# Kernel tuning notes

Hardware: AMD Instinct MI355X
Metric: run time of the kernel (lower is better)

The kernel has to match this reference:

```python
import jax, jax.numpy as jnp
import numpy as np

SEQ, D_IN, D_OUT = 8192, 1024, 1024

def setup_inputs() -> dict:
    key = jax.random.key(0)
    kx, kq, kk, kv = jax.random.split(key, 4)
    scale = 1.0 / np.sqrt(D_IN)
    return {
        "x": jax.random.normal(kx, (SEQ, D_IN), dtype=jnp.float32),
        "Wq": jax.random.normal(kq, (D_OUT, D_IN), dtype=jnp.float32) * scale,
        "Wk": jax.random.normal(kk, (D_OUT, D_IN), dtype=jnp.float32) * scale,
        "Wv": jax.random.normal(kv, (D_OUT, D_IN), dtype=jnp.float32) * scale,
    }

def reference(x, Wq, Wk, Wv):
    # nn.Linear: y = x @ W.T (no bias)
    q = x @ Wq.T            # [S, d_out]
    k = x @ Wk.T            # [S, d_out]
    v = x @ Wv.T            # [S, d_out]
    d_k = k.shape[-1]
    scores = (q @ k.T) / jnp.sqrt(jnp.float32(d_k))   # [S, S]
    attn = jax.nn.softmax(scores, axis=-1)
    return attn @ v         # [S, d_out]
```

## Files before the change

### kernel.cpp

```cpp
#include <hip/hip_runtime.h>

typedef unsigned short ushort_t;
typedef __attribute__((ext_vector_type(8))) __bf16 bf16x8;
typedef __attribute__((ext_vector_type(4))) float f32x4;

#define SEQ 8192
#define DIN 1024
#define DOUT 1024

#define OM_BF16 0
#define OM_F32  1
#define OM_EXP  2
#define OM_NORM 3

__device__ __forceinline__ ushort_t f2bf(float f) {
  union { float f; unsigned u; } c; c.f = f;
  unsigned u = c.u;
  return (ushort_t)((u + 0x7fffu + ((u >> 16) & 1u)) >> 16);
}

__device__ __forceinline__ void async16(ushort_t* lds, const ushort_t* g) {
  __builtin_amdgcn_global_load_lds(
      (__attribute__((address_space(1))) void*)g,
      (__attribute__((address_space(3))) void*)lds, 16, 0, 0);
}

__global__ __launch_bounds__(256) void cvt_all_kernel(
    const float* __restrict__ x, const float* __restrict__ wq,
    const float* __restrict__ wk, const float* __restrict__ wv,
    ushort_t* __restrict__ xb, ushort_t* __restrict__ wqkb,
    ushort_t* __restrict__ wvb) {
  int b = blockIdx.x;
  const float* src;
  ushort_t* dst;
  int idx;
  if (b < 8192) {
    src = x; dst = xb; idx = b * 256 + threadIdx.x;
  } else {
    int r = b - 8192;
    int w = r >> 10;
    idx = (r & 1023) * 256 + threadIdx.x;
    if (w == 0)      { src = wq; dst = wqkb; }
    else if (w == 1) { src = wk; dst = wqkb + DOUT * DIN; }
    else             { src = wv; dst = wvb; }
  }
  float4 f = ((const float4*)src)[idx];
  ushort4 o;
  o.x = f2bf(f.x); o.y = f2bf(f.y); o.z = f2bf(f.z); o.w = f2bf(f.w);
  ((ushort4*)dst)[idx] = o;
}

__global__ __launch_bounds__(256) void rowsum_inv_kernel(const float* __restrict__ rsp,
                                                         float* __restrict__ invrs) {
  int r = blockIdx.x * 256 + threadIdx.x;
  float s = 0.f;
  #pragma unroll
  for (int p2 = 0; p2 < 64; ++p2) s += rsp[p2 * SEQ + r];
  invrs[r] = 1.0f / s;
}

template <int OUTMODE, int SWZ, int BK>
__global__ __launch_bounds__(256) void gemm_bt(const ushort_t* __restrict__ A,
                                               const ushort_t* __restrict__ B,
                                               void* __restrict__ C,
                                               int lda, int ldb, int ldc,
                                               int K, float scale,
                                               float* __restrict__ rsp,
                                               const float* __restrict__ invrs) {
  constexpr int CPR = BK / 8;
  constexpr int NI = BK / 16;
  __shared__ ushort_t As[128 * BK];
  __shared__ ushort_t Bs[128 * BK];
  const int t = threadIdx.x;
  const int lane = t & 63;
  const int wave = t >> 6;
  const int wr = wave >> 1, wc = wave & 1;
  const int quad = lane >> 4, r16 = lane & 15;

  int mt, nt;
  if (SWZ == 1) {
    mt = blockIdx.x * (gridDim.y >> 3) + (blockIdx.y >> 3);
    nt = blockIdx.y & 7;
  } else {
    mt = blockIdx.y;
    nt = blockIdx.x;
  }
  const int rowBase = mt * 128;
  const int colBase = nt * 128;

  unsigned offA[NI], offB[NI];
  #pragma unroll
  for (int i = 0; i < NI; ++i) {
    int c = t + i * 256;
    int row = c / CPR;
    int kq = c & (CPR - 1);
    int kqs = (kq & ~7) | ((kq & 7) ^ (row & 7));
    offA[i] = (unsigned)((rowBase + row) * lda + kqs * 8);
    offB[i] = (unsigned)((colBase + row) * ldb + kqs * 8);
  }

  f32x4 acc[4][4] = {};

  const int nk = K / BK;
  for (int kt = 0; kt < nk; ++kt) {
    #pragma unroll
    for (int i = 0; i < NI; ++i) {
      async16(&As[(t + i * 256) * 8], A + offA[i]); offA[i] += BK;
      async16(&Bs[(t + i * 256) * 8], B + offB[i]); offB[i] += BK;
    }
    __syncthreads();
    #pragma unroll
    for (int ks = 0; ks < BK / 32; ++ks) {
      bf16x8 af[4], bfr[4];
      #pragma unroll
      for (int mi = 0; mi < 4; ++mi) {
        int row = wr * 64 + mi * 16 + r16;
        int kq = ks * 4 + quad;
        int c = row * CPR + ((kq & ~7) | ((kq & 7) ^ (row & 7)));
        af[mi] = *(const bf16x8*)&As[c * 8];
      }
      #pragma unroll
      for (int ni = 0; ni < 4; ++ni) {
        int row = wc * 64 + ni * 16 + r16;
        int kq = ks * 4 + quad;
        int c = row * CPR + ((kq & ~7) | ((kq & 7) ^ (row & 7)));
        bfr[ni] = *(const bf16x8*)&Bs[c * 8];
      }
      #pragma unroll
      for (int mi = 0; mi < 4; ++mi)
        #pragma unroll
        for (int ni = 0; ni < 4; ++ni)
          acc[mi][ni] = __builtin_amdgcn_mfma_f32_16x16x32_bf16(af[mi], bfr[ni],
                                                                acc[mi][ni], 0, 0, 0);
    }
    __syncthreads();
  }

  float iv[4][4];
  if (OUTMODE == OM_NORM) {
    #pragma unroll
    for (int mi = 0; mi < 4; ++mi)
      #pragma unroll
      for (int r = 0; r < 4; ++r)
        iv[mi][r] = invrs[rowBase + wr * 64 + mi * 16 + quad * 4 + r];
  }

  float psum[4][4];
  if (OUTMODE == OM_EXP) {
    #pragma unroll
    for (int mi = 0; mi < 4; ++mi)
      #pragma unroll
      for (int r = 0; r < 4; ++r) psum[mi][r] = 0.f;
  }

  #pragma unroll
  for (int mi = 0; mi < 4; ++mi)
    #pragma unroll
    for (int ni = 0; ni < 4; ++ni)
      #pragma unroll
      for (int r = 0; r < 4; ++r) {
        int grow = rowBase + wr * 64 + mi * 16 + quad * 4 + r;
        int gcol = colBase + wc * 64 + ni * 16 + r16;
        float a = acc[mi][ni][r];
        if (OUTMODE == OM_F32) {
          ((float*)C)[(size_t)grow * ldc + gcol] = a * scale;
        } else if (OUTMODE == OM_BF16) {
          ((ushort_t*)C)[(size_t)grow * ldc + gcol] = f2bf(a * scale);
        } else if (OUTMODE == OM_EXP) {
          float e = exp2f(a * scale);
          psum[mi][r] += e;
          ((ushort_t*)C)[(size_t)grow * ldc + gcol] = f2bf(e);
        } else {
          ((float*)C)[(size_t)grow * ldc + gcol] = a * iv[mi][r];
        }
      }

  if (OUTMODE == OM_EXP) {
    float* lds_rs = (float*)As;
    #pragma unroll
    for (int mi = 0; mi < 4; ++mi)
      #pragma unroll
      for (int r = 0; r < 4; ++r) {
        float s = psum[mi][r];
        s += __shfl_xor(s, 1, 64);
        s += __shfl_xor(s, 2, 64);
        s += __shfl_xor(s, 4, 64);
        s += __shfl_xor(s, 8, 64);
        if (r16 == 0)
          lds_rs[wc * 128 + wr * 64 + mi * 16 + quad * 4 + r] = s;
      }
    __syncthreads();
    if (t < 128)
      rsp[(size_t)nt * SEQ + rowBase + t] = lds_rs[t] + lds_rs[128 + t];
  }
}

extern "C" void kernel_launch(void* const* d_in, const int* in_sizes, int n_in,
                              void* d_out, int out_size, void* d_ws, size_t ws_size,
                              hipStream_t stream) {
  const float* x  = (const float*)d_in[0];
  const float* Wq = (const float*)d_in[1];
  const float* Wk = (const float*)d_in[2];
  const float* Wv = (const float*)d_in[3];
  float* out = (float*)d_out;

  char* p = (char*)d_ws;
  ushort_t* xb   = (ushort_t*)p; p += (size_t)SEQ * DIN * 2;
  ushort_t* wqkb = (ushort_t*)p; p += (size_t)2 * DOUT * DIN * 2;
  ushort_t* wvb  = (ushort_t*)p; p += (size_t)DOUT * DIN * 2;
  ushort_t* qkb  = (ushort_t*)p; p += (size_t)SEQ * 2 * DOUT * 2;
  ushort_t* vtb  = (ushort_t*)p; p += (size_t)DOUT * SEQ * 2;
  float*    rsp  = (float*)p;    p += (size_t)64 * SEQ * 4;
  float*    irs  = (float*)p;    p += (size_t)SEQ * 4;
  ushort_t* Sb   = (ushort_t*)p; p += (size_t)SEQ * SEQ * 2;

  cvt_all_kernel<<<8192 + 3 * 1024, 256, 0, stream>>>(x, Wq, Wk, Wv, xb, wqkb, wvb);

  dim3 blk(256);
  gemm_bt<OM_BF16, 0, 64><<<dim3(2048 / 128, SEQ / 128), blk, 0, stream>>>(
      xb, wqkb, qkb, DIN, DIN, 2 * DOUT, DIN, 1.0f, nullptr, nullptr);

  gemm_bt<OM_BF16, 0, 128><<<dim3(SEQ / 128, DOUT / 128), blk, 0, stream>>>(
      wvb, xb, vtb, DIN, DIN, SEQ, DIN, 1.0f, nullptr, nullptr);

  gemm_bt<OM_EXP, 0, 64><<<dim3(SEQ / 128, SEQ / 128), blk, 0, stream>>>(
      qkb, qkb + DOUT, Sb, 2 * DOUT, 2 * DOUT, SEQ, DIN,
      0.03125f * 1.44269504f, rsp, nullptr);

  rowsum_inv_kernel<<<SEQ / 256, blk, 0, stream>>>(rsp, irs);

  gemm_bt<OM_NORM, 1, 128><<<dim3(DOUT / 128, SEQ / 128), blk, 0, stream>>>(
      Sb, vtb, out, SEQ, SEQ, DOUT, SEQ, 1.0f, nullptr, irs);
}
```

Before: 478.0 us.

## Merge QK and V projections into one launch, use packed bf16 conversion

Merges the two projection GEMMs (QK and transposed V) into a single launch of 1536 blocks. The V projection now uses BK=64 instead of 128. Bf16 conversion uses the hardware packed cvt instruction where available, both in the input cast kernel and in the GEMM epilogues. The epilogue loop is restructured so the row multiplier is computed once per row. The aim is to remove one launch and its tail, and to cut the ALU cost of the bf16 rounding. Stores stay scalar 16-bit, and rounding behaviour may differ slightly.

```diff
diff --git a/kernel.cpp b/kernel.cpp
--- a/kernel.cpp
+++ b/kernel.cpp
@@ -13,10 +13,30 @@
 #define OM_EXP  2
 #define OM_NORM 3
 
+#if defined(__has_builtin)
+#if __has_builtin(__builtin_amdgcn_cvt_pk_bf16_f32)
+#define HAVE_PK_BF16 1
+#endif
+#endif
+#ifndef HAVE_PK_BF16
+#define HAVE_PK_BF16 0
+#endif
+
 __device__ __forceinline__ ushort_t f2bf(float f) {
   union { float f; unsigned u; } c; c.f = f;
   unsigned u = c.u;
   return (ushort_t)((u + 0x7fffu + ((u >> 16) & 1u)) >> 16);
+}
+
+__device__ __forceinline__ unsigned pk_bf16(float a, float b) {
+#if HAVE_PK_BF16
+  auto r = __builtin_amdgcn_cvt_pk_bf16_f32(a, b);
+  unsigned u;
+  __builtin_memcpy(&u, &r, 4);
+  return u;
+#else
+  return (unsigned)f2bf(a) | ((unsigned)f2bf(b) << 16);
+#endif
 }
 
 __device__ __forceinline__ void async16(ushort_t* lds, const ushort_t* g) {
@@ -45,9 +65,10 @@
     else             { src = wv; dst = wvb; }
   }
   float4 f = ((const float4*)src)[idx];
-  ushort4 o;
-  o.x = f2bf(f.x); o.y = f2bf(f.y); o.z = f2bf(f.z); o.w = f2bf(f.w);
-  ((ushort4*)dst)[idx] = o;
+  unsigned u01 = pk_bf16(f.x, f.y);
+  unsigned u23 = pk_bf16(f.z, f.w);
+  uint2 o; o.x = u01; o.y = u23;
+  ((uint2*)dst)[idx] = o;
 }
 
 __global__ __launch_bounds__(256) void rowsum_inv_kernel(const float* __restrict__ rsp,
@@ -59,32 +80,24 @@
   invrs[r] = 1.0f / s;
 }
 
-template <int OUTMODE, int SWZ, int BK>
-__global__ __launch_bounds__(256) void gemm_bt(const ushort_t* __restrict__ A,
-                                               const ushort_t* __restrict__ B,
-                                               void* __restrict__ C,
-                                               int lda, int ldb, int ldc,
-                                               int K, float scale,
-                                               float* __restrict__ rsp,
-                                               const float* __restrict__ invrs) {
+template <int OUTMODE, int BK>
+__device__ __forceinline__ void gemm_body(const ushort_t* __restrict__ A,
+                                          const ushort_t* __restrict__ B,
+                                          void* __restrict__ C,
+                                          int lda, int ldb, int ldc,
+                                          int K, float scale,
+                                          float* __restrict__ rsp,
+                                          const float* __restrict__ invrs,
+                                          int mt, int nt,
+                                          ushort_t* As, ushort_t* Bs) {
   constexpr int CPR = BK / 8;
   constexpr int NI = BK / 16;
-  __shared__ ushort_t As[128 * BK];
-  __shared__ ushort_t Bs[128 * BK];
   const int t = threadIdx.x;
   const int lane = t & 63;
   const int wave = t >> 6;
   const int wr = wave >> 1, wc = wave & 1;
   const int quad = lane >> 4, r16 = lane & 15;
 
-  int mt, nt;
-  if (SWZ == 1) {
-    mt = blockIdx.x * (gridDim.y >> 3) + (blockIdx.y >> 3);
-    nt = blockIdx.y & 7;
-  } else {
-    mt = blockIdx.y;
-    nt = blockIdx.x;
-  }
   const int rowBase = mt * 128;
   const int colBase = nt * 128;
 
@@ -156,24 +169,32 @@
   #pragma unroll
   for (int mi = 0; mi < 4; ++mi)
     #pragma unroll
-    for (int ni = 0; ni < 4; ++ni)
-      #pragma unroll
-      for (int r = 0; r < 4; ++r) {
-        int grow = rowBase + wr * 64 + mi * 16 + quad * 4 + r;
-        int gcol = colBase + wc * 64 + ni * 16 + r16;
-        float a = acc[mi][ni][r];
-        if (OUTMODE == OM_F32) {
-          ((float*)C)[(size_t)grow * ldc + gcol] = a * scale;
-        } else if (OUTMODE == OM_BF16) {
-          ((ushort_t*)C)[(size_t)grow * ldc + gcol] = f2bf(a * scale);
-        } else if (OUTMODE == OM_EXP) {
-          float e = exp2f(a * scale);
-          psum[mi][r] += e;
-          ((ushort_t*)C)[(size_t)grow * ldc + gcol] = f2bf(e);
-        } else {
-          ((float*)C)[(size_t)grow * ldc + gcol] = a * iv[mi][r];
+    for (int r = 0; r < 4; ++r) {
+      int grow = rowBase + wr * 64 + mi * 16 + quad * 4 + r;
+      if (OUTMODE == OM_F32 || OUTMODE == OM_NORM) {
+        float m = (OUTMODE == OM_NORM) ? iv[mi][r] : scale;
+        #pragma unroll
+        for (int ni = 0; ni < 4; ++ni) {
+          int gcol = colBase + wc * 64 + ni * 16 + r16;
+          ((float*)C)[(size_t)grow * ldc + gcol] = acc[mi][ni][r] * m;
         }
-      }
+      } else {
+        float e[4];
+        #pragma unroll
+        for (int ni = 0; ni < 4; ++ni) {
+          float a = acc[mi][ni][r] * scale;
+          if (OUTMODE == OM_EXP) { a = exp2f(a); psum[mi][r] += a; }
+          e[ni] = a;
+        }
+        unsigned u01 = pk_bf16(e[0], e[1]);
+        unsigned u23 = pk_bf16(e[2], e[3]);
+        ushort_t* cp = (ushort_t*)C + (size_t)grow * ldc + colBase + wc * 64 + r16;
+        cp[0]  = (ushort_t)u01;
+        cp[16] = (ushort_t)(u01 >> 16);
+        cp[32] = (ushort_t)u23;
+        cp[48] = (ushort_t)(u23 >> 16);
+      }
+    }
 
   if (OUTMODE == OM_EXP) {
     float* lds_rs = (float*)As;
@@ -193,6 +214,49 @@
     if (t < 128)
       rsp[(size_t)nt * SEQ + rowBase + t] = lds_rs[t] + lds_rs[128 + t];
   }
+}
+
+template <int OUTMODE, int SWZ, int BK>
+__global__ __launch_bounds__(256) void gemm_bt(const ushort_t* __restrict__ A,
+                                               const ushort_t* __restrict__ B,
+                                               void* __restrict__ C,
+                                               int lda, int ldb, int ldc,
+                                               int K, float scale,
+                                               float* __restrict__ rsp,
+                                               const float* __restrict__ invrs) {
+  __shared__ ushort_t As[128 * BK];
+  __shared__ ushort_t Bs[128 * BK];
+  int mt, nt;
+  if (SWZ == 1) {
+    mt = blockIdx.x * (gridDim.y >> 3) + (blockIdx.y >> 3);
+    nt = blockIdx.y & 7;
+  } else {
+    mt = blockIdx.y;
+    nt = blockIdx.x;
+  }
+  gemm_body<OUTMODE, BK>(A, B, C, lda, ldb, ldc, K, scale, rsp, invrs, mt, nt, As, Bs);
+}
+
+__global__ __launch_bounds__(256) void proj_fused_kernel(
+    const ushort_t* __restrict__ xb, const ushort_t* __restrict__ wqkb,
+    const ushort_t* __restrict__ wvb, ushort_t* __restrict__ qkb,
+    ushort_t* __restrict__ vtb) {
+  __shared__ ushort_t As[128 * 64];
+  __shared__ ushort_t Bs[128 * 64];
+  int b = blockIdx.x;
+  const ushort_t *A, *B;
+  ushort_t* C;
+  int ldc, mt, nt;
+  if (b < 1024) {
+    A = xb; B = wqkb; C = qkb; ldc = 2 * DOUT;
+    mt = b >> 4; nt = b & 15;
+  } else {
+    int b2 = b - 1024;
+    A = wvb; B = xb; C = vtb; ldc = SEQ;
+    mt = b2 >> 6; nt = b2 & 63;
+  }
+  gemm_body<OM_BF16, 64>(A, B, C, DIN, DIN, ldc, DIN, 1.0f, nullptr, nullptr,
+                         mt, nt, As, Bs);
 }
 
 extern "C" void kernel_launch(void* const* d_in, const int* in_sizes, int n_in,
@@ -217,11 +281,7 @@
   cvt_all_kernel<<<8192 + 3 * 1024, 256, 0, stream>>>(x, Wq, Wk, Wv, xb, wqkb, wvb);
 
   dim3 blk(256);
-  gemm_bt<OM_BF16, 0, 64><<<dim3(2048 / 128, SEQ / 128), blk, 0, stream>>>(
-      xb, wqkb, qkb, DIN, DIN, 2 * DOUT, DIN, 1.0f, nullptr, nullptr);
-
-  gemm_bt<OM_BF16, 0, 128><<<dim3(SEQ / 128, DOUT / 128), blk, 0, stream>>>(
-      wvb, xb, vtb, DIN, DIN, SEQ, DIN, 1.0f, nullptr, nullptr);
+  proj_fused_kernel<<<1536, blk, 0, stream>>>(xb, wqkb, wvb, qkb, vtb);
 
   gemm_bt<OM_EXP, 0, 64><<<dim3(SEQ / 128, SEQ / 128), blk, 0, stream>>>(
       qkb, qkb + DOUT, Sb, 2 * DOUT, 2 * DOUT, SEQ, DIN,
```

Result: no change. 484.2 us (+1.3%).
